# Optimization experiments

Hardware: AMD Instinct MI355X
Metric: run time of the kernel (lower is better)

The kernel has to match this reference:

```python
import jax, jax.numpy as jnp
import numpy as np

N_NODES = 8192
IN_F = 256
OUT_F = 256
ALPHA = 0.2  # LeakyReLU negative slope


def setup_inputs() -> dict:
    key = jax.random.key(0)
    k1, k2, k3, k4 = jax.random.split(key, 4)
    X = jax.random.normal(k1, (N_NODES, IN_F), dtype=jnp.float32)
    A = jax.random.randint(k2, (N_NODES, N_NODES), 0, 2, dtype=jnp.int32)
    # torch nn.Linear weight layout: (out_features, in_features)
    W = jax.random.normal(k3, (OUT_F, IN_F), dtype=jnp.float32) * (1.0 / np.sqrt(IN_F))
    r = jax.random.normal(k4, (2 * OUT_F, 1), dtype=jnp.float32)
    return {"X": X, "A": A, "W": W, "r": r}


def reference(X, A, W, r):
    # Wh = X @ W^T  -> (N, F_out)
    Wh = X @ W.T
    # Split r so that cat([Wh_i, Wh_j]) @ r == Wh_i @ r_src + Wh_j @ r_dst
    F_out = Wh.shape[-1]
    r_src = r[:F_out, 0]   # (F,)
    r_dst = r[F_out:, 0]   # (F,)
    s_i = Wh @ r_src       # (N,)
    s_j = Wh @ r_dst       # (N,)
    e = s_i[:, None] + s_j[None, :]                      # (N, N)
    e = jnp.where(e >= 0, e, ALPHA * e)                  # LeakyReLU
    e = jnp.where(A == 0, -jnp.inf, e)                   # mask non-edges
    attention = jax.nn.softmax(e, axis=1)                # row-wise softmax
    output = attention @ Wh                              # (N, F_out)
    return jax.nn.gelu(output, approximate=False)        # torch F.gelu (exact)
```

## Files before the change

### kernel.cpp

```cpp
#include <hip/hip_runtime.h>
#include <hip/hip_bf16.h>

#define N_NODES 8192
#define NF      256
#define L2E     1.44269504088896341f

typedef __attribute__((ext_vector_type(8))) short short8;
typedef __attribute__((ext_vector_type(4))) short short4v;
typedef __attribute__((ext_vector_type(4))) float floatx4;

static __device__ __forceinline__ float bf2f(short s) {
    return __uint_as_float(((unsigned)(unsigned short)s) << 16);
}
static __device__ __forceinline__ short f2bf_rn(float f) {
    unsigned u = __float_as_uint(f) + 0x8000u;
    return (short)(u >> 16);
}
struct bfpair { short hi, lo; };
static __device__ __forceinline__ bfpair split_bf(float x) {
    bfpair p;
    p.hi = f2bf_rn(x);
    p.lo = f2bf_rn(x - bf2f(p.hi));
    return p;
}
static __device__ __forceinline__ void async16(const void* g, void* l) {
    __builtin_amdgcn_global_load_lds(
        (const __attribute__((address_space(1))) unsigned*)g,
        (__attribute__((address_space(3))) unsigned*)l, 16, 0, 0);
}

__global__ __launch_bounds__(256) void kx_split(const float* __restrict__ W,
                                                short* __restrict__ Whi,
                                                short* __restrict__ Wlo) {
    #pragma unroll
    for (int e = 0; e < 4; ++e) {
        const int i = blockIdx.x * 1024 + e * 256 + threadIdx.x;
        bfpair p = split_bf(W[i]);
        Whi[i] = p.hi;
        Wlo[i] = p.lo;
    }
}

__global__ __launch_bounds__(512) void k1_gemm(const float* __restrict__ X,
                                               const short* __restrict__ Whi,
                                               const short* __restrict__ Wlo,
                                               const float* __restrict__ r,
                                               short* __restrict__ WhT,
                                               float* __restrict__ sp_src,
                                               float* __restrict__ sp_dst) {
    __shared__ float Xs[32 * 256];

    const int tid = threadIdx.x;
    const int w = tid >> 6, lane = tid & 63;
    const int q = lane >> 4, m = lane & 15;
    const int rh = w >> 2, cq = w & 3;
    const int i_base = blockIdx.x * 32;

    #pragma unroll
    for (int v = 0; v < 4; ++v) {
        const int rowv = w * 4 + v;
        const int c = lane ^ (rowv & 7);
        async16(X + (size_t)(i_base + rowv) * NF + c * 4, &Xs[rowv * 256]);
    }
    __syncthreads();

    floatx4 acc[4] = {};
    const int xrow = rh * 16 + m;
    const int r7 = xrow & 7;
    #pragma unroll
    for (int ks = 0; ks < 8; ++ks) {
        const int c0 = ks * 8 + q * 2;
        float4 f0 = *(const float4*)(&Xs[xrow * 256 + ((c0 ^ r7) * 4)]);
        float4 f1 = *(const float4*)(&Xs[xrow * 256 + (((c0 + 1) ^ r7) * 4)]);
        const float xsv[8] = {f0.x, f0.y, f0.z, f0.w, f1.x, f1.y, f1.z, f1.w};
        short8 xh, xl;
        #pragma unroll
        for (int c = 0; c < 8; ++c) {
            bfpair p = split_bf(xsv[c]);
            xh[c] = p.hi; xl[c] = p.lo;
        }
        #pragma unroll
        for (int nt = 0; nt < 4; ++nt) {
            const int n = cq * 64 + nt * 16 + m;
            short8 wh = *(const short8*)(Whi + n * NF + ks * 32 + q * 8);
            short8 wl = *(const short8*)(Wlo + n * NF + ks * 32 + q * 8);
            acc[nt] = __builtin_amdgcn_mfma_f32_16x16x32_bf16(xh, wh, acc[nt], 0, 0, 0);
            acc[nt] = __builtin_amdgcn_mfma_f32_16x16x32_bf16(xl, wh, acc[nt], 0, 0, 0);
            acc[nt] = __builtin_amdgcn_mfma_f32_16x16x32_bf16(xh, wl, acc[nt], 0, 0, 0);
        }
    }

    const int i0 = i_base + rh * 16 + q * 4;
    float vs[4] = {0.f, 0.f, 0.f, 0.f}, vd[4] = {0.f, 0.f, 0.f, 0.f};
    #pragma unroll
    for (int nt = 0; nt < 4; ++nt) {
        const int n = cq * 64 + nt * 16 + m;
        short4v v;
        #pragma unroll
        for (int r2 = 0; r2 < 4; ++r2) v[r2] = f2bf_rn(acc[nt][r2]);
        *(short4v*)(WhT + (size_t)n * N_NODES + i0) = v;
        const float rs = r[n], rd = r[NF + n];
        #pragma unroll
        for (int r2 = 0; r2 < 4; ++r2) {
            vs[r2] = fmaf(acc[nt][r2], rs, vs[r2]);
            vd[r2] = fmaf(acc[nt][r2], rd, vd[r2]);
        }
    }
    #pragma unroll
    for (int mask = 1; mask <= 8; mask <<= 1) {
        #pragma unroll
        for (int r2 = 0; r2 < 4; ++r2) {
            vs[r2] += __shfl_xor(vs[r2], mask);
            vd[r2] += __shfl_xor(vd[r2], mask);
        }
    }
    if (m == 0) {
        #pragma unroll
        for (int r2 = 0; r2 < 4; ++r2) {
            sp_src[cq * N_NODES + i0 + r2] = vs[r2];
            sp_dst[cq * N_NODES + i0 + r2] = vd[r2];
        }
    }
}

__global__ __launch_bounds__(256) void k2_sv(const float* __restrict__ sp_src,
                                             const float* __restrict__ sp_dst,
                                             float* __restrict__ s_src,
                                             float* __restrict__ s_dst,
                                             float* __restrict__ pmax) {
    __shared__ float red[256];
    const int tid = threadIdx.x;
    const int i = blockIdx.x * 256 + tid;
    float ss = 0.f, sd = 0.f;
    #pragma unroll
    for (int nb = 0; nb < 4; ++nb) {
        ss += sp_src[nb * N_NODES + i];
        sd += sp_dst[nb * N_NODES + i];
    }
    s_src[i] = ss;
    s_dst[i] = sd;
    red[tid] = sd;
    __syncthreads();
    for (int off = 128; off > 0; off >>= 1) {
        if (tid < off) red[tid] = fmaxf(red[tid], red[tid + off]);
        __syncthreads();
    }
    if (tid == 0) pmax[blockIdx.x] = red[0];
}

static __device__ __forceinline__ void pgroup(const int4 a, const floatx4 t,
                                              const float s_i, const float d_i,
                                              float* p) {
    const int av[4] = {a.x, a.y, a.z, a.w};
    #pragma unroll
    for (int c = 0; c < 4; ++c) {
        float sum = s_i + t[c];
        float lr  = fmaxf(sum, 0.2f * sum);
        float pp  = __builtin_amdgcn_exp2f(fmaf(lr, L2E, d_i));
        p[c] = (av[c] != 0) ? pp : 0.0f;
    }
}

__global__ __launch_bounds__(1024) void k4_attn(const int* __restrict__ Adj,
                                                const short* __restrict__ WhT,
                                                const float* __restrict__ s_dst,
                                                const float* __restrict__ s_src,
                                                const float* __restrict__ pmax,
                                                float* __restrict__ out) {
    __shared__ union {
        short B[2][256][128];
        float red[16 * 8 * 4 * 64];
    } sm;
    __shared__ float denred[128];

    const int tid = threadIdx.x;
    const int w = tid >> 6, lane = tid & 63;
    const int q = lane >> 4, m = lane & 15;
    const int rh = w >> 3, ch = (w >> 2) & 1, jq = w & 3;
    const int i0 = blockIdx.x * 32;
    const int row = i0 + rh * 16 + m;

    float M = pmax[0];
    #pragma unroll
    for (int b = 1; b < 32; ++b) M = fmaxf(M, pmax[b]);
    const float s_i = s_src[row];
    const float e0 = s_i + M;
    const float d_i = -fmaxf(e0, 0.2f * e0) * L2E;

    const int nloc = lane >> 4;
    const int scl = lane & 15;
    const short* gB[4];
    #pragma unroll
    for (int v = 0; v < 4; ++v) {
        const int n = w * 16 + v * 4 + nloc;
        const int c = scl ^ (n & 7);
        gB[v] = WhT + (size_t)n * N_NODES + c * 8;
    }

    const int* Ap = Adj + (size_t)row * N_NODES + jq * 32 + q * 8;
    const float* tp = s_dst + jq * 32 + q * 8;

    floatx4 acc[8];
    #pragma unroll
    for (int nt = 0; nt < 8; ++nt) acc[nt] = (floatx4){0.f, 0.f, 0.f, 0.f};
    float den = 0.f;

    #pragma unroll
    for (int v = 0; v < 4; ++v)
        async16(gB[v], &sm.B[0][w * 16 + v * 4][0]);
    int4 a0 = *(const int4*)(Ap);
    int4 a1 = *(const int4*)(Ap + 4);
    floatx4 t0 = *(const floatx4*)(tp);
    floatx4 t1 = *(const floatx4*)(tp + 4);
    __syncthreads();

    for (int s = 0; s < 64; ++s) {
        const int cur = s & 1;

        short* dstb = &sm.B[cur ^ 1][0][0];
        const int go = ((s + 1) & 63) * 128;
        #pragma unroll
        for (int v = 0; v < 4; ++v)
            async16(gB[v] + go, dstb + (w * 16 + v * 4) * 128);
        __builtin_amdgcn_sched_barrier(0);

        int4 na0 = *(const int4*)(Ap + go);
        int4 na1 = *(const int4*)(Ap + go + 4);
        floatx4 nt0 = *(const floatx4*)(tp + go);
        floatx4 nt1 = *(const floatx4*)(tp + go + 4);
        __builtin_amdgcn_sched_barrier(0);

        float p[8];
        pgroup(a0, t0, s_i, d_i, p);
        pgroup(a1, t1, s_i, d_i, p + 4);

        short8 af;
        #pragma unroll
        for (int c = 0; c < 8; ++c) af[c] = f2bf_rn(p[c]);
        #pragma unroll
        for (int c = 0; c < 8; ++c) den += p[c];

        const short* Bb = &sm.B[cur][0][0];
        __builtin_amdgcn_s_setprio(1);
        #pragma unroll
        for (int nt = 0; nt < 8; ++nt) {
            const int n = ch * 128 + nt * 16 + m;
            const int sc = (jq * 4 + q) ^ (n & 7);
            short8 b0 = *(const short8*)(Bb + n * 128 + sc * 8);
            acc[nt] = __builtin_amdgcn_mfma_f32_16x16x32_bf16(af, b0, acc[nt], 0, 0, 0);
        }
        __builtin_amdgcn_s_setprio(0);

        __builtin_amdgcn_sched_barrier(0);
        asm volatile("s_waitcnt vmcnt(4)" ::: "memory");
        __builtin_amdgcn_s_barrier();

        a0 = na0; a1 = na1; t0 = nt0; t1 = nt1;
    }

    den += __shfl_xor(den, 16);
    den += __shfl_xor(den, 32);
    if (ch == 0 && lane < 16) denred[rh * 64 + jq * 16 + lane] = den;
    #pragma unroll
    for (int nt = 0; nt < 8; ++nt)
        #pragma unroll
        for (int rg = 0; rg < 4; ++rg)
            sm.red[((w * 8 + nt) * 4 + rg) * 64 + lane] = acc[nt][rg];
    __syncthreads();

    float invd[4];
    #pragma unroll
    for (int rg = 0; rg < 4; ++rg) {
        const int rr = rh * 64 + q * 4 + rg;
        invd[rg] = 1.0f / fmaxf(denred[rr] + denred[rr + 16] +
                                denred[rr + 32] + denred[rr + 48], 1e-30f);
    }
    const int wb = rh * 8 + ch * 4;
    #pragma unroll
    for (int t2 = 0; t2 < 2; ++t2) {
        const int nt = jq * 2 + t2;
        #pragma unroll
        for (int rg = 0; rg < 4; ++rg) {
            float v = sm.red[(((wb + 0) * 8 + nt) * 4 + rg) * 64 + lane]
                    + sm.red[(((wb + 1) * 8 + nt) * 4 + rg) * 64 + lane]
                    + sm.red[(((wb + 2) * 8 + nt) * 4 + rg) * 64 + lane]
                    + sm.red[(((wb + 3) * 8 + nt) * 4 + rg) * 64 + lane];
            float x = v * invd[rg];
            float g = 0.5f * x * (1.0f + erff(x * 0.70710678118f));
            out[(size_t)(i0 + rh * 16 + q * 4 + rg) * NF + ch * 128 + nt * 16 + m] = g;
        }
    }
}

extern "C" void kernel_launch(void* const* d_in, const int* in_sizes, int n_in,
                              void* d_out, int out_size, void* d_ws, size_t ws_size,
                              hipStream_t stream) {
    const float* X = (const float*)d_in[0];
    const int*   A = (const int*)d_in[1];
    const float* W = (const float*)d_in[2];
    const float* r = (const float*)d_in[3];
    float* out = (float*)d_out;

    char* wsp = (char*)d_ws;
    short* WhT    = (short*)wsp;                    wsp += (size_t)NF * N_NODES * 2;
    short* Whi    = (short*)wsp;                    wsp += NF * NF * 2;
    short* Wlo    = (short*)wsp;                    wsp += NF * NF * 2;
    float* sp_src = (float*)wsp;                    wsp += 4 * N_NODES * 4;
    float* sp_dst = (float*)wsp;                    wsp += 4 * N_NODES * 4;
    float* s_src  = (float*)wsp;                    wsp += N_NODES * 4;
    float* s_dst  = (float*)wsp;                    wsp += N_NODES * 4;
    float* pmax   = (float*)wsp;

    kx_split<<<64, 256, 0, stream>>>(W, Whi, Wlo);
    k1_gemm<<<256, 512, 0, stream>>>(X, Whi, Wlo, r, WhT, sp_src, sp_dst);
    k2_sv<<<32, 256, 0, stream>>>(sp_src, sp_dst, s_src, s_dst, pmax);
    k4_attn<<<256, 1024, 0, stream>>>(A, WhT, s_dst, s_src, pmax, out);
}
```

Baseline: 479.0 us.

## Split attention kernel across output-feature halves to double block count

The attention kernel now launches 512 blocks, each computing 128 of the 256 output features for a 32-row tile, instead of 256 blocks covering all features. This halves the shared-memory B tile and the accumulator registers per block, which may let more blocks reside per CU and fill all CUs. The cost is that each half recomputes the masked exponentials and re-reads the full adjacency rows, doubling reads of the 256 MB int32 adjacency matrix.

```diff
diff --git a/kernel.cpp b/kernel.cpp
--- a/kernel.cpp
+++ b/kernel.cpp
@@ -161,23 +161,26 @@
     }
 }
 
-__global__ __launch_bounds__(1024) void k4_attn(const int* __restrict__ Adj,
-                                                const short* __restrict__ WhT,
-                                                const float* __restrict__ s_dst,
-                                                const float* __restrict__ s_src,
-                                                const float* __restrict__ pmax,
-                                                float* __restrict__ out) {
+__global__ __launch_bounds__(1024, 8) void k4_attn(const int* __restrict__ Adj,
+                                                   const short* __restrict__ WhT,
+                                                   const float* __restrict__ s_dst,
+                                                   const float* __restrict__ s_src,
+                                                   const float* __restrict__ pmax,
+                                                   float* __restrict__ out) {
     __shared__ union {
-        short B[2][256][128];
-        float red[16 * 8 * 4 * 64];
+        short B[2][128][128];
+        float red[16 * 4 * 4 * 64];
     } sm;
     __shared__ float denred[128];
 
     const int tid = threadIdx.x;
     const int w = tid >> 6, lane = tid & 63;
     const int q = lane >> 4, m = lane & 15;
-    const int rh = w >> 3, ch = (w >> 2) & 1, jq = w & 3;
-    const int i0 = blockIdx.x * 32;
+    const int rh = w >> 3, nhw = (w >> 2) & 1, jq = w & 3;
+    const int ib = blockIdx.x & 255;
+    const int nh = blockIdx.x >> 8;
+    const int i0 = ib * 32;
+    const int n_base = nh * 128;
     const int row = i0 + rh * 16 + m;
 
     float M = pmax[0];
@@ -189,25 +192,25 @@
 
     const int nloc = lane >> 4;
     const int scl = lane & 15;
-    const short* gB[4];
-    #pragma unroll
-    for (int v = 0; v < 4; ++v) {
-        const int n = w * 16 + v * 4 + nloc;
-        const int c = scl ^ (n & 7);
-        gB[v] = WhT + (size_t)n * N_NODES + c * 8;
+    const short* gB[2];
+    #pragma unroll
+    for (int v = 0; v < 2; ++v) {
+        const int nl = w * 8 + v * 4 + nloc;
+        const int c = scl ^ (nl & 7);
+        gB[v] = WhT + (size_t)(n_base + nl) * N_NODES + c * 8;
     }
 
     const int* Ap = Adj + (size_t)row * N_NODES + jq * 32 + q * 8;
     const float* tp = s_dst + jq * 32 + q * 8;
 
-    floatx4 acc[8];
-    #pragma unroll
-    for (int nt = 0; nt < 8; ++nt) acc[nt] = (floatx4){0.f, 0.f, 0.f, 0.f};
+    floatx4 acc[4];
+    #pragma unroll
+    for (int nt = 0; nt < 4; ++nt) acc[nt] = (floatx4){0.f, 0.f, 0.f, 0.f};
     float den = 0.f;
 
     #pragma unroll
-    for (int v = 0; v < 4; ++v)
-        async16(gB[v], &sm.B[0][w * 16 + v * 4][0]);
+    for (int v = 0; v < 2; ++v)
+        async16(gB[v], &sm.B[0][w * 8 + v * 4][0]);
     int4 a0 = *(const int4*)(Ap);
     int4 a1 = *(const int4*)(Ap + 4);
     floatx4 t0 = *(const floatx4*)(tp);
@@ -220,8 +223,8 @@
         short* dstb = &sm.B[cur ^ 1][0][0];
         const int go = ((s + 1) & 63) * 128;
         #pragma unroll
-        for (int v = 0; v < 4; ++v)
-            async16(gB[v] + go, dstb + (w * 16 + v * 4) * 128);
+        for (int v = 0; v < 2; ++v)
+            async16(gB[v] + go, dstb + (w * 8 + v * 4) * 128);
         __builtin_amdgcn_sched_barrier(0);
 
         int4 na0 = *(const int4*)(Ap + go);
@@ -243,10 +246,10 @@
         const short* Bb = &sm.B[cur][0][0];
         __builtin_amdgcn_s_setprio(1);
         #pragma unroll
-        for (int nt = 0; nt < 8; ++nt) {
-            const int n = ch * 128 + nt * 16 + m;
-            const int sc = (jq * 4 + q) ^ (n & 7);
-            short8 b0 = *(const short8*)(Bb + n * 128 + sc * 8);
+        for (int nt = 0; nt < 4; ++nt) {
+            const int nl = nhw * 64 + nt * 16 + m;
+            const int sc = (jq * 4 + q) ^ (nl & 7);
+            short8 b0 = *(const short8*)(Bb + nl * 128 + sc * 8);
             acc[nt] = __builtin_amdgcn_mfma_f32_16x16x32_bf16(af, b0, acc[nt], 0, 0, 0);
         }
         __builtin_amdgcn_s_setprio(0);
@@ -260,12 +263,12 @@
 
     den += __shfl_xor(den, 16);
     den += __shfl_xor(den, 32);
-    if (ch == 0 && lane < 16) denred[rh * 64 + jq * 16 + lane] = den;
-    #pragma unroll
-    for (int nt = 0; nt < 8; ++nt)
+    if (nhw == 0 && lane < 16) denred[rh * 64 + jq * 16 + lane] = den;
+    #pragma unroll
+    for (int nt = 0; nt < 4; ++nt)
         #pragma unroll
         for (int rg = 0; rg < 4; ++rg)
-            sm.red[((w * 8 + nt) * 4 + rg) * 64 + lane] = acc[nt][rg];
+            sm.red[((w * 4 + nt) * 4 + rg) * 64 + lane] = acc[nt][rg];
     __syncthreads();
 
     float invd[4];
@@ -275,19 +278,18 @@
         invd[rg] = 1.0f / fmaxf(denred[rr] + denred[rr + 16] +
                                 denred[rr + 32] + denred[rr + 48], 1e-30f);
     }
-    const int wb = rh * 8 + ch * 4;
-    #pragma unroll
-    for (int t2 = 0; t2 < 2; ++t2) {
-        const int nt = jq * 2 + t2;
+    const int wb = rh * 8 + nhw * 4;
+    {
+        const int nt = jq;
         #pragma unroll
         for (int rg = 0; rg < 4; ++rg) {
-            float v = sm.red[(((wb + 0) * 8 + nt) * 4 + rg) * 64 + lane]
-                    + sm.red[(((wb + 1) * 8 + nt) * 4 + rg) * 64 + lane]
-                    + sm.red[(((wb + 2) * 8 + nt) * 4 + rg) * 64 + lane]
-                    + sm.red[(((wb + 3) * 8 + nt) * 4 + rg) * 64 + lane];
+            float v = sm.red[(((wb + 0) * 4 + nt) * 4 + rg) * 64 + lane]
+                    + sm.red[(((wb + 1) * 4 + nt) * 4 + rg) * 64 + lane]
+                    + sm.red[(((wb + 2) * 4 + nt) * 4 + rg) * 64 + lane]
+                    + sm.red[(((wb + 3) * 4 + nt) * 4 + rg) * 64 + lane];
             float x = v * invd[rg];
             float g = 0.5f * x * (1.0f + erff(x * 0.70710678118f));
-            out[(size_t)(i0 + rh * 16 + q * 4 + rg) * NF + ch * 128 + nt * 16 + m] = g;
+            out[(size_t)(i0 + rh * 16 + q * 4 + rg) * NF + n_base + nhw * 64 + nt * 16 + m] = g;
         }
     }
 }
@@ -314,5 +316,5 @@
     kx_split<<<64, 256, 0, stream>>>(W, Whi, Wlo);
     k1_gemm<<<256, 512, 0, stream>>>(X, Whi, Wlo, r, WhT, sp_src, sp_dst);
     k2_sv<<<32, 256, 0, stream>>>(sp_src, sp_dst, s_src, s_dst, pmax);
-    k4_attn<<<256, 1024, 0, stream>>>(A, WhT, s_dst, s_src, pmax, out);
-}
+    k4_attn<<<512, 1024, 0, stream>>>(A, WhT, s_dst, s_src, pmax, out);
+}
```

Measured after the change: 528.1 us. 10.3% more time.

## Split attention over two column halves with atomic accumulation and a finalize kernel

Applied to the files above, without the earlier changes.

The attention kernel now splits the 8192 neighbor columns into two halves, launching 512 blocks of 512 threads instead of 256 blocks of 1024. Each block accumulates its partial numerator into the zeroed output with atomicAdd and writes a partial denominator. A new finalize kernel sums the two denominators, normalizes, and applies GELU. This aims to improve occupancy and CU coverage on the 256-CU part, at the cost of a memset, global atomics, an extra launch and a second pass over the output.

```diff
diff --git a/kernel.cpp b/kernel.cpp
--- a/kernel.cpp
+++ b/kernel.cpp
@@ -161,23 +161,27 @@
     }
 }
 
-__global__ __launch_bounds__(1024) void k4_attn(const int* __restrict__ Adj,
-                                                const short* __restrict__ WhT,
-                                                const float* __restrict__ s_dst,
-                                                const float* __restrict__ s_src,
-                                                const float* __restrict__ pmax,
-                                                float* __restrict__ out) {
+__global__ __launch_bounds__(512, 4) void k4_attn(const int* __restrict__ Adj,
+                                                  const short* __restrict__ WhT,
+                                                  const float* __restrict__ s_dst,
+                                                  const float* __restrict__ s_src,
+                                                  const float* __restrict__ pmax,
+                                                  float* __restrict__ pden,
+                                                  float* __restrict__ outacc) {
     __shared__ union {
-        short B[2][256][128];
-        float red[16 * 8 * 4 * 64];
+        short B[2][256][64];
+        float red[8 * 8 * 4 * 64];
     } sm;
-    __shared__ float denred[128];
+    __shared__ float denred[64];
 
     const int tid = threadIdx.x;
     const int w = tid >> 6, lane = tid & 63;
     const int q = lane >> 4, m = lane & 15;
-    const int rh = w >> 3, ch = (w >> 2) & 1, jq = w & 3;
-    const int i0 = blockIdx.x * 32;
+    const int rh = w >> 2, ch = (w >> 1) & 1, jq = w & 1;
+    const int ib = blockIdx.x & 255;
+    const int jh = blockIdx.x >> 8;
+    const int i0 = ib * 32;
+    const int jbase = jh * 4096;
     const int row = i0 + rh * 16 + m;
 
     float M = pmax[0];
@@ -187,18 +191,15 @@
     const float e0 = s_i + M;
     const float d_i = -fmaxf(e0, 0.2f * e0) * L2E;
 
-    const int nloc = lane >> 4;
-    const int scl = lane & 15;
+    const int srow = lane >> 3;
+    const int scc = (lane & 7) ^ srow;
     const short* gB[4];
     #pragma unroll
-    for (int v = 0; v < 4; ++v) {
-        const int n = w * 16 + v * 4 + nloc;
-        const int c = scl ^ (n & 7);
-        gB[v] = WhT + (size_t)n * N_NODES + c * 8;
-    }
-
-    const int* Ap = Adj + (size_t)row * N_NODES + jq * 32 + q * 8;
-    const float* tp = s_dst + jq * 32 + q * 8;
+    for (int v = 0; v < 4; ++v)
+        gB[v] = WhT + (size_t)(w * 32 + v * 8 + srow) * N_NODES + jbase + scc * 8;
+
+    const int* Ap = Adj + (size_t)row * N_NODES + jbase + jq * 32 + q * 8;
+    const float* tp = s_dst + jbase + jq * 32 + q * 8;
 
     floatx4 acc[8];
     #pragma unroll
@@ -207,7 +208,7 @@
 
     #pragma unroll
     for (int v = 0; v < 4; ++v)
-        async16(gB[v], &sm.B[0][w * 16 + v * 4][0]);
+        async16(gB[v], &sm.B[0][w * 32 + v * 8][0]);
     int4 a0 = *(const int4*)(Ap);
     int4 a1 = *(const int4*)(Ap + 4);
     floatx4 t0 = *(const floatx4*)(tp);
@@ -218,10 +219,10 @@
         const int cur = s & 1;
 
         short* dstb = &sm.B[cur ^ 1][0][0];
-        const int go = ((s + 1) & 63) * 128;
+        const int go = ((s + 1) & 63) * 64;
         #pragma unroll
         for (int v = 0; v < 4; ++v)
-            async16(gB[v] + go, dstb + (w * 16 + v * 4) * 128);
+            async16(gB[v] + go, dstb + (w * 32 + v * 8) * 64);
         __builtin_amdgcn_sched_barrier(0);
 
         int4 na0 = *(const int4*)(Ap + go);
@@ -245,8 +246,8 @@
         #pragma unroll
         for (int nt = 0; nt < 8; ++nt) {
             const int n = ch * 128 + nt * 16 + m;
-            const int sc = (jq * 4 + q) ^ (n & 7);
-            short8 b0 = *(const short8*)(Bb + n * 128 + sc * 8);
+            const int sc = (jq * 4 + q) ^ (m & 7);
+            short8 b0 = *(const short8*)(Bb + n * 64 + sc * 8);
             acc[nt] = __builtin_amdgcn_mfma_f32_16x16x32_bf16(af, b0, acc[nt], 0, 0, 0);
         }
         __builtin_amdgcn_s_setprio(0);
@@ -260,7 +261,7 @@
 
     den += __shfl_xor(den, 16);
     den += __shfl_xor(den, 32);
-    if (ch == 0 && lane < 16) denred[rh * 64 + jq * 16 + lane] = den;
+    if (ch == 0 && lane < 16) denred[rh * 32 + jq * 16 + lane] = den;
     #pragma unroll
     for (int nt = 0; nt < 8; ++nt)
         #pragma unroll
@@ -268,28 +269,44 @@
             sm.red[((w * 8 + nt) * 4 + rg) * 64 + lane] = acc[nt][rg];
     __syncthreads();
 
-    float invd[4];
-    #pragma unroll
-    for (int rg = 0; rg < 4; ++rg) {
-        const int rr = rh * 64 + q * 4 + rg;
-        invd[rg] = 1.0f / fmaxf(denred[rr] + denred[rr + 16] +
-                                denred[rr + 32] + denred[rr + 48], 1e-30f);
-    }
-    const int wb = rh * 8 + ch * 4;
-    #pragma unroll
-    for (int t2 = 0; t2 < 2; ++t2) {
-        const int nt = jq * 2 + t2;
-        #pragma unroll
-        for (int rg = 0; rg < 4; ++rg) {
-            float v = sm.red[(((wb + 0) * 8 + nt) * 4 + rg) * 64 + lane]
-                    + sm.red[(((wb + 1) * 8 + nt) * 4 + rg) * 64 + lane]
-                    + sm.red[(((wb + 2) * 8 + nt) * 4 + rg) * 64 + lane]
-                    + sm.red[(((wb + 3) * 8 + nt) * 4 + rg) * 64 + lane];
-            float x = v * invd[rg];
-            float g = 0.5f * x * (1.0f + erff(x * 0.70710678118f));
-            out[(size_t)(i0 + rh * 16 + q * 4 + rg) * NF + ch * 128 + nt * 16 + m] = g;
-        }
-    }
+    if (w == 0 && lane < 32) {
+        const int rr = lane >> 4, mm = lane & 15;
+        pden[jh * N_NODES + i0 + rr * 16 + mm] =
+            denred[rr * 32 + mm] + denred[rr * 32 + 16 + mm];
+    }
+    if (jq == 0) {
+        #pragma unroll
+        for (int nt = 0; nt < 8; ++nt) {
+            #pragma unroll
+            for (int rg = 0; rg < 4; ++rg) {
+                float v = sm.red[((w * 8 + nt) * 4 + rg) * 64 + lane]
+                        + sm.red[(((w + 1) * 8 + nt) * 4 + rg) * 64 + lane];
+                const int orow = i0 + rh * 16 + q * 4 + rg;
+                const int n = ch * 128 + nt * 16 + m;
+                atomicAdd(&outacc[(size_t)orow * NF + n], v);
+            }
+        }
+    }
+}
+
+__global__ __launch_bounds__(256) void k5_fin(const float* __restrict__ pden,
+                                              float* __restrict__ out) {
+    const int gid = blockIdx.x * 256 + threadIdx.x;
+    const int row = gid >> 5;
+    const int c0 = (gid & 31) * 8;
+    const float d = pden[row] + pden[N_NODES + row];
+    const float inv = 1.0f / fmaxf(d, 1e-30f);
+    float* p = out + (size_t)row * NF + c0;
+    float4 v0 = *(const float4*)(p);
+    float4 v1 = *(const float4*)(p + 4);
+    float xs[8] = {v0.x, v0.y, v0.z, v0.w, v1.x, v1.y, v1.z, v1.w};
+    #pragma unroll
+    for (int c = 0; c < 8; ++c) {
+        const float x = xs[c] * inv;
+        xs[c] = 0.5f * x * (1.0f + erff(x * 0.70710678118f));
+    }
+    *(float4*)(p)     = (float4){xs[0], xs[1], xs[2], xs[3]};
+    *(float4*)(p + 4) = (float4){xs[4], xs[5], xs[6], xs[7]};
 }
 
 extern "C" void kernel_launch(void* const* d_in, const int* in_sizes, int n_in,
@@ -310,9 +327,12 @@
     float* s_src  = (float*)wsp;                    wsp += N_NODES * 4;
     float* s_dst  = (float*)wsp;                    wsp += N_NODES * 4;
     float* pmax   = (float*)wsp;
-
+    float* pden   = sp_src;
+
+    hipMemsetAsync(out, 0, (size_t)N_NODES * NF * 4, stream);
     kx_split<<<64, 256, 0, stream>>>(W, Whi, Wlo);
     k1_gemm<<<256, 512, 0, stream>>>(X, Whi, Wlo, r, WhT, sp_src, sp_dst);
     k2_sv<<<32, 256, 0, stream>>>(sp_src, sp_dst, s_src, s_dst, pmax);
-    k4_attn<<<256, 1024, 0, stream>>>(A, WhT, s_dst, s_src, pmax, out);
-}
+    k4_attn<<<512, 512, 0, stream>>>(A, WhT, s_dst, s_src, pmax, pden, out);
+    k5_fin<<<1024, 256, 0, stream>>>(pden, out);
+}
```

After: 478.9 us. No clear change (-0.0%).
